# Optimization experiments

Measured on AMD Instinct MI355X. Metric: run time of the kernel, lower is better.

## Reference

```python
import jax, jax.numpy as jnp
import numpy as np

B, H, W, DIM = 32, 56, 56, 192
WSZ = 7
HEADS = 8
DK = 32
DV = 32
INNER_K = HEADS * DK  # 256
INNER_V = HEADS * DV  # 256


def setup_inputs() -> dict:
    key = jax.random.key(0)
    ks = jax.random.split(key, 8)
    s = 0.05
    return {
        "x": jax.random.normal(ks[0], (B, H, W, DIM), jnp.float32),
        "Wq": jax.random.normal(ks[1], (DIM, INNER_K), jnp.float32) * s,
        "Wk": jax.random.normal(ks[2], (DIM, INNER_K), jnp.float32) * s,
        "Wv": jax.random.normal(ks[3], (DIM, INNER_V), jnp.float32) * s,
        "Wlocal": jax.random.normal(ks[4], (3, 3, INNER_V, INNER_V), jnp.float32) * s,
        "b_local": jnp.zeros((INNER_V,), jnp.float32),
        "Wout": jax.random.normal(ks[5], (INNER_V, DIM), jnp.float32) * s,
        "b_out": jnp.zeros((DIM,), jnp.float32),
    }


def _window(t, heads, wsz):
    # (b, H, W, heads*d) -> (b*nx*ny, heads, wsz*wsz, d)
    b, h, w, c = t.shape
    d = c // heads
    nx, ny = h // wsz, w // wsz
    t = t.reshape(b, nx, wsz, ny, wsz, heads, d)
    t = t.transpose(0, 1, 3, 5, 2, 4, 6)
    return t.reshape(b * nx * ny, heads, wsz * wsz, d)


def reference(x, Wq, Wk, Wv, Wlocal, b_local, Wout, b_out):
    scale = DK ** (-0.5)
    # 1x1 convs == per-pixel matmuls
    q = jnp.einsum('bhwc,cd->bhwd', x, Wq)
    k = jnp.einsum('bhwc,cd->bhwd', x, Wk)
    v = jnp.einsum('bhwc,cd->bhwd', x, Wv)
    # 3x3 local interactive conv on v (SAME padding)
    local_out = jax.lax.conv_general_dilated(
        v, Wlocal, window_strides=(1, 1), padding='SAME',
        dimension_numbers=('NHWC', 'HWIO', 'NHWC')) + b_local
    # window partition
    qw = _window(q, HEADS, WSZ)
    kw = _window(k, HEADS, WSZ)
    vw = _window(v, HEADS, WSZ)
    dots = jnp.einsum('bhid,bhjd->bhij', qw, kw) * scale  # (B*nx*ny, heads, 49, 49)
    attn = jax.nn.softmax(dots, axis=-1)
    out = jnp.einsum('bhij,bhjd->bhid', attn, vw)
    # window merge: (b*nx*ny, heads, wsz*wsz, d) -> (b, H, W, heads*d)
    nx, ny = H // WSZ, W // WSZ
    out = out.reshape(B, nx, ny, HEADS, WSZ, WSZ, DV)
    out = out.transpose(0, 1, 4, 2, 5, 3, 6).reshape(B, H, W, HEADS * DV)
    out = out + local_out
    out = jnp.einsum('bhwc,cd->bhwd', out, Wout) + b_out
    return out
```

## Files before the change

### kernel.cpp

```cpp
#include <hip/hip_runtime.h>

typedef unsigned short ushort_t;
typedef __bf16  bf16x8 __attribute__((ext_vector_type(8)));
typedef float   f32x4  __attribute__((ext_vector_type(4)));
typedef unsigned short u16x8 __attribute__((ext_vector_type(8)));

#define MFMA16(a,b,c) __builtin_amdgcn_mfma_f32_16x16x32_bf16((a),(b),(c),0,0,0)
#define WAITVM(N) asm volatile("s_waitcnt vmcnt(" #N ")" ::: "memory")
#define BARRIER() do{ __builtin_amdgcn_s_barrier(); asm volatile("" ::: "memory"); }while(0)

static __device__ __forceinline__ ushort_t f2bf(float f){
  __bf16 h = (__bf16)f;
  return __builtin_bit_cast(ushort_t, h);
}
static __device__ __forceinline__ float bf2f(ushort_t b){
  union{unsigned u; float f;} x; x.u = ((unsigned)b)<<16; return x.f;
}
static __device__ __forceinline__ bf16x8 ldg_bf8u(const ushort_t* p){
  u16x8 r = *(const u16x8*)p;
  return __builtin_bit_cast(bf16x8, r);
}
static __device__ __forceinline__ bf16x8 lds_bf8(const ushort_t* p){
  u16x8 r = *(const u16x8*)p;
  return __builtin_bit_cast(bf16x8, r);
}
static __device__ __forceinline__ void gload_lds16(const ushort_t* g, ushort_t* l){
  __builtin_amdgcn_global_load_lds(
      (const __attribute__((address_space(1))) void*)g,
      (__attribute__((address_space(3))) void*)l, 16, 0, 0);
}

__global__ __launch_bounds__(256) void prep_kernel(
    const float* __restrict__ Wq, const float* __restrict__ Wk,
    const float* __restrict__ Wv, const float* __restrict__ Wl,
    const float* __restrict__ Wo,
    ushort_t* __restrict__ qkvT, ushort_t* __restrict__ wlT,
    ushort_t* __restrict__ woT)
{
  int idx = blockIdx.x*256 + threadIdx.x;
  if(idx < 147456){
    int n = idx/192, kk = idx%192;
    const float* W = (n < 256) ? Wq : ((n < 512) ? Wk : Wv);
    qkvT[idx] = f2bf(W[kk*256 + (n & 255)]);
  } else if(idx < 147456 + 589824){
    int t2 = idx - 147456;
    int j   = t2 & 7;
    int sl  = (t2 >> 3) & 3;
    int col = (t2 >> 5) & 255;
    int ks  = (t2 >> 13) & 7;
    int tap = t2 >> 16;
    int grp = sl ^ ((col>>1)&3);
    int k = ks*32 + grp*8 + j;
    wlT[t2] = f2bf(Wl[((size_t)tap*256 + k)*256 + col]);
  } else if(idx < 737280 + 49152){
    int t3 = idx - 737280;
    int col = t3/256, kk = t3%256;
    woT[t3] = f2bf(Wo[kk*192 + col]);
  }
}

__global__ __launch_bounds__(512) void qkvattn_kernel(
    const float* __restrict__ x, const ushort_t* __restrict__ WT,
    ushort_t* __restrict__ vbuf, ushort_t* __restrict__ attnout)
{
  __shared__ ushort_t lds[53248];
  ushort_t* xLds = lds;
  const int tid = threadIdx.x;
  const int w = tid>>6, l = tid&63, lr = l&15, g = l>>4;
  const int win = blockIdx.x;
  const int b = win>>6, rem = win&63, wy = rem>>3, wx = rem&7;
  const size_t base = (size_t)b*3136 + wy*7*56 + wx*7;

  #pragma unroll
  for(int r=0;r<3;++r){
    int c = tid + r*512;
    int row = c/24, cp = c%24;
    u16x8 o = {0,0,0,0,0,0,0,0};
    if(row < 49){
      int sc = cp ^ (row&7);
      const float* src = x + (base + (row/7)*56 + (row%7))*192 + sc*8;
      float4 f0 = *(const float4*)src;
      float4 f1 = *(const float4*)(src+4);
      o[0]=f2bf(f0.x); o[1]=f2bf(f0.y); o[2]=f2bf(f0.z); o[3]=f2bf(f0.w);
      o[4]=f2bf(f1.x); o[5]=f2bf(f1.y); o[6]=f2bf(f1.z); o[7]=f2bf(f1.w);
    }
    *(u16x8*)&xLds[row*192 + cp*8] = o;
  }
  __syncthreads();

  ushort_t* qkBase = lds + 16384 + w*4608;
  ushort_t* vT     = lds + w*2048;
  #pragma unroll
  for(int which=0; which<3; ++which){
    const ushort_t* Wb = WT + (size_t)(which*256 + w*32)*192;
    f32x4 acc[4][2];
    #pragma unroll
    for(int mi=0;mi<4;++mi)
      #pragma unroll
      for(int nj=0;nj<2;++nj){ f32x4 z={0.f,0.f,0.f,0.f}; acc[mi][nj]=z; }
    bf16x8 bA[2], bB[2];
    #pragma unroll
    for(int nj=0;nj<2;++nj) bA[nj] = ldg_bf8u(Wb + (size_t)(nj*16+lr)*192 + g*8);
    #pragma unroll
    for(int ks2=0; ks2<3; ++ks2){
      int ks0 = 2*ks2, ks1 = 2*ks2+1;
      #pragma unroll
      for(int nj=0;nj<2;++nj) bB[nj] = ldg_bf8u(Wb + (size_t)(nj*16+lr)*192 + ks1*32 + g*8);
      #pragma unroll
      for(int mi=0;mi<4;++mi){
        int row = mi*16 + lr;
        bf16x8 af = lds_bf8(&xLds[(row*192 + ks0*32 + g*8) ^ ((row&7)<<3)]);
        #pragma unroll
        for(int nj=0;nj<2;++nj) acc[mi][nj] = MFMA16(af, bA[nj], acc[mi][nj]);
      }
      if(ks2<2){
        #pragma unroll
        for(int nj=0;nj<2;++nj) bA[nj] = ldg_bf8u(Wb + (size_t)(nj*16+lr)*192 + (ks1+1)*32 + g*8);
      }
      #pragma unroll
      for(int mi=0;mi<4;++mi){
        int row = mi*16 + lr;
        bf16x8 af = lds_bf8(&xLds[(row*192 + ks1*32 + g*8) ^ ((row&7)<<3)]);
        #pragma unroll
        for(int nj=0;nj<2;++nj) acc[mi][nj] = MFMA16(af, bB[nj], acc[mi][nj]);
      }
    }
    if(which < 2){
      ushort_t* dst = qkBase + which*2304;
      #pragma unroll
      for(int mi=0;mi<4;++mi)
        #pragma unroll
        for(int nj=0;nj<2;++nj)
          #pragma unroll
          for(int i=0;i<4;++i){
            int row = mi*16 + g*4 + i, col = nj*16 + lr;
            dst[row*36 + col] = f2bf(acc[mi][nj][i]);
          }
    } else {
      __syncthreads();
      #pragma unroll
      for(int mi=0;mi<4;++mi)
        #pragma unroll
        for(int nj=0;nj<2;++nj)
          #pragma unroll
          for(int i=0;i<4;++i){
            int row = mi*16 + g*4 + i, col = nj*16 + lr;
            ushort_t val = f2bf(acc[mi][nj][i]);
            vT[(col*64 + row) ^ ((col&7)<<3)] = val;
            if(row < 49)
              vbuf[(base + (row/7)*56 + (row%7))*256 + w*32 + col] = val;
          }
    }
  }

  f32x4 dot[4][4];
  #pragma unroll
  for(int mi=0;mi<4;++mi)
    #pragma unroll
    for(int nj=0;nj<4;++nj){ f32x4 z={0.f,0.f,0.f,0.f}; dot[mi][nj]=z; }
  bf16x8 qf[4], kf[4];
  #pragma unroll
  for(int t=0;t<4;++t){
    qf[t] = lds_bf8(&qkBase[(t*16+lr)*36 + g*8]);
    kf[t] = lds_bf8(&qkBase[2304 + (t*16+lr)*36 + g*8]);
  }
  #pragma unroll
  for(int mi=0;mi<4;++mi)
    #pragma unroll
    for(int nj=0;nj<4;++nj)
      dot[mi][nj] = MFMA16(qf[mi], kf[nj], dot[mi][nj]);
  const float sc = 0.17677669529663687f * 1.4426950408889634f;
  ushort_t* pl = qkBase;
  float rs[4][4];
  #pragma unroll
  for(int mi=0;mi<4;++mi){
    #pragma unroll
    for(int i=0;i<4;++i){
      float m = -1e30f;
      #pragma unroll
      for(int nj=0;nj<4;++nj){
        int col = nj*16 + lr;
        if(col < 49) m = fmaxf(m, dot[mi][nj][i]);
      }
      m = fmaxf(m, __shfl_xor(m,1));
      m = fmaxf(m, __shfl_xor(m,2));
      m = fmaxf(m, __shfl_xor(m,4));
      m = fmaxf(m, __shfl_xor(m,8));
      float e[4]; float s = 0.f;
      #pragma unroll
      for(int nj=0;nj<4;++nj){
        int col = nj*16 + lr;
        e[nj] = (col < 49) ? exp2f((dot[mi][nj][i]-m)*sc) : 0.f;
        s += e[nj];
      }
      s += __shfl_xor(s,1); s += __shfl_xor(s,2);
      s += __shfl_xor(s,4); s += __shfl_xor(s,8);
      rs[mi][i] = s;
      int row = mi*16 + g*4 + i;
      #pragma unroll
      for(int nj=0;nj<4;++nj){
        int col = nj*16 + lr;
        pl[(row*64 + col) ^ ((row&7)<<3)] = f2bf(e[nj]);
      }
    }
  }
  f32x4 o[4][2];
  #pragma unroll
  for(int mi=0;mi<4;++mi)
    #pragma unroll
    for(int nj=0;nj<2;++nj){ f32x4 z={0.f,0.f,0.f,0.f}; o[mi][nj]=z; }
  #pragma unroll
  for(int ks=0;ks<2;++ks){
    bf16x8 pa[4];
    #pragma unroll
    for(int mi=0;mi<4;++mi){
      int row = mi*16 + lr;
      pa[mi] = lds_bf8(&pl[(row*64 + ks*32 + g*8) ^ ((row&7)<<3)]);
    }
    #pragma unroll
    for(int nj=0;nj<2;++nj){
      int d = nj*16 + lr;
      bf16x8 vb = lds_bf8(&vT[(d*64 + ks*32 + g*8) ^ ((d&7)<<3)]);
      #pragma unroll
      for(int mi=0;mi<4;++mi) o[mi][nj] = MFMA16(pa[mi], vb, o[mi][nj]);
    }
  }
  #pragma unroll
  for(int mi=0;mi<4;++mi){
    #pragma unroll
    for(int i=0;i<4;++i){
      int row = mi*16 + g*4 + i;
      if(row < 49){
        size_t pix = base + (row/7)*56 + (row%7);
        float inv = 1.0f / rs[mi][i];
        #pragma unroll
        for(int nj=0;nj<2;++nj)
          attnout[pix*256 + w*32 + nj*16 + lr] = f2bf(o[mi][nj][i] * inv);
      }
    }
  }
}

__global__ __launch_bounds__(256,2) void conv_kernel(
    const ushort_t* __restrict__ v, const ushort_t* __restrict__ WlT,
    const float* __restrict__ b_local, ushort_t* __restrict__ local_out)
{
  __shared__ ushort_t aBuf[2][256*32];
  __shared__ ushort_t bBuf[3][256*32];
  const int bid = blockIdx.x;
  const int tile = (bid & 7) * 98 + (bid >> 3);
  const int p0 = tile * 128;
  const int tid = threadIdx.x;
  const int l = tid&63, w=tid>>6, wm=w>>1, wn=w&1, lr=l&15, g=l>>4;

  unsigned maskbits[4];
  int pxloc[4];
  #pragma unroll
  for(int mi=0;mi<4;++mi){
    int p = p0 + wm*64 + mi*16 + lr;
    int rem = p % 3136;
    int y = rem/56, x = rem%56;
    unsigned mb = 0;
    #pragma unroll
    for(int tap=0;tap<9;++tap){
      int dy = tap/3 - 1, dx = tap%3 - 1;
      if(((unsigned)(y+dy) < 56u) && ((unsigned)(x+dx) < 56u)) mb |= (1u<<tap);
    }
    maskbits[mi] = mb;
    pxloc[mi] = wm*64 + mi*16 + lr + 64;
  }

  auto stageA = [&](int ks, ushort_t* dst){
    #pragma unroll
    for(int r=0;r<4;++r){
      int c = tid + r*256;
      int px = c>>2, sl = c&3;
      int px_abs = p0 - 64 + px;
      px_abs = min(max(px_abs, 0), 100351);
      int chunk = sl ^ ((px>>1)&3);
      gload_lds16(v + (size_t)px_abs*256 + ks*32 + chunk*8,
                  dst + (size_t)(r*256 + w*64)*8);
    }
  };
  auto stageB = [&](int ks, int tap, ushort_t* dst){
    const ushort_t* src = WlT + ((size_t)tap*8 + ks)*8192;
    #pragma unroll
    for(int r=0;r<4;++r){
      gload_lds16(src + (size_t)(tid + r*256)*8,
                  dst + (size_t)(r*256 + w*64)*8);
    }
  };

  f32x4 acc[4][8];
  #pragma unroll
  for(int mi=0;mi<4;++mi)
    #pragma unroll
    for(int nj=0;nj<8;++nj){ f32x4 z={0.f,0.f,0.f,0.f}; acc[mi][nj]=z; }

  auto compute = [&](int tap, const ushort_t* aL, const ushort_t* bL){
    int shift = (tap/3 - 1)*56 + (tap%3 - 1);
    bf16x8 af[4];
    #pragma unroll
    for(int mi=0;mi<4;++mi){
      int px = pxloc[mi] + shift;
      int sl = g ^ ((px>>1)&3);
      u16x8 rv = *(const u16x8*)&aL[px*32 + sl*8];
      if(!((maskbits[mi]>>tap)&1)){ u16x8 z={0,0,0,0,0,0,0,0}; rv=z; }
      af[mi] = __builtin_bit_cast(bf16x8, rv);
    }
    __builtin_amdgcn_s_setprio(1);
    #pragma unroll
    for(int nj=0;nj<8;++nj){
      int col = wn*128 + nj*16 + lr;
      int slb = g ^ ((col>>1)&3);
      bf16x8 bfr = lds_bf8(&bL[col*32 + slb*8]);
      #pragma unroll
      for(int mi=0;mi<4;++mi) acc[mi][nj] = MFMA16(af[mi], bfr, acc[mi][nj]);
    }
    __builtin_amdgcn_s_setprio(0);
  };

  stageA(0, aBuf[0]);
  stageB(0, 0, bBuf[0]);
  stageB(0, 1, bBuf[1]);

  for(int ks=0; ks<7; ++ks){
    #pragma unroll
    for(int tap=0; tap<9; ++tap){
      if(tap==1) WAITVM(8); else WAITVM(4);
      BARRIER();
      if(tap==0) stageA(ks+1, aBuf[(ks+1)&1]);
      stageB(ks + (tap+2)/9, (tap+2)%9, bBuf[(tap+2)%3]);
      compute(tap, aBuf[ks&1], bBuf[tap%3]);
    }
  }
  #pragma unroll
  for(int tap=0; tap<9; ++tap){
    if(tap==8) WAITVM(0); else WAITVM(4);
    BARRIER();
    if(tap<7) stageB(7, tap+2, bBuf[(tap+2)%3]);
    compute(tap, aBuf[1], bBuf[tap%3]);
  }

  #pragma unroll
  for(int nj=0;nj<8;++nj){
    int col = wn*128 + nj*16 + lr;
    float bb = b_local[col];
    #pragma unroll
    for(int mi=0;mi<4;++mi)
      #pragma unroll
      for(int i=0;i<4;++i){
        int p = p0 + wm*64 + mi*16 + g*4 + i;
        local_out[(size_t)p*256 + col] = f2bf(acc[mi][nj][i] + bb);
      }
  }
}

__global__ __launch_bounds__(256,4) void outproj_kernel(
    const ushort_t* __restrict__ attnout, const ushort_t* __restrict__ locl,
    const ushort_t* __restrict__ WoT, const float* __restrict__ b_out,
    float* __restrict__ out)
{
  __shared__ ushort_t aLds[64*256];
  const int m0 = blockIdx.x * 64;
  const int tid = threadIdx.x;
  const int l = tid&63, w = tid>>6, lr=l&15, g=l>>4;
  #pragma unroll
  for(int r=0;r<8;++r){
    int c = tid + r*256;
    int row = c>>5, cc = c&31;
    size_t off = (size_t)(m0+row)*256 + cc*8;
    u16x8 a = *(const u16x8*)(attnout + off);
    u16x8 b2 = *(const u16x8*)(locl + off);
    u16x8 o;
    #pragma unroll
    for(int j=0;j<8;++j) o[j] = f2bf(bf2f(a[j]) + bf2f(b2[j]));
    *(u16x8*)&aLds[(row*256 + cc*8) ^ ((row&7)<<3)] = o;
  }
  __syncthreads();

  const ushort_t* Wbase = WoT + (size_t)(w*48)*256;
  f32x4 acc[4][3];
  #pragma unroll
  for(int mi=0;mi<4;++mi)
    #pragma unroll
    for(int nj=0;nj<3;++nj){ f32x4 z={0.f,0.f,0.f,0.f}; acc[mi][nj]=z; }

  #pragma unroll
  for(int ks=0;ks<8;++ks){
    bf16x8 bfr[3];
    #pragma unroll
    for(int nj=0;nj<3;++nj)
      bfr[nj] = ldg_bf8u(Wbase + (size_t)(nj*16+lr)*256 + ks*32 + g*8);
    bf16x8 af[4];
    #pragma unroll
    for(int mi=0;mi<4;++mi){
      int row = mi*16 + lr;
      af[mi] = lds_bf8(&aLds[(row*256 + ks*32 + g*8) ^ ((row&7)<<3)]);
    }
    #pragma unroll
    for(int nj=0;nj<3;++nj)
      #pragma unroll
      for(int mi=0;mi<4;++mi) acc[mi][nj] = MFMA16(af[mi], bfr[nj], acc[mi][nj]);
  }
  #pragma unroll
  for(int nj=0;nj<3;++nj){
    int col = w*48 + nj*16 + lr;
    float bb = b_out[col];
    #pragma unroll
    for(int mi=0;mi<4;++mi)
      #pragma unroll
      for(int i=0;i<4;++i){
        int row = mi*16 + g*4 + i;
        out[(size_t)(m0+row)*192 + col] = acc[mi][nj][i] + bb;
      }
  }
}

extern "C" void kernel_launch(void* const* d_in, const int* in_sizes, int n_in,
                              void* d_out, int out_size, void* d_ws, size_t ws_size,
                              hipStream_t stream)
{
  const float* x  = (const float*)d_in[0];
  const float* Wq = (const float*)d_in[1];
  const float* Wk = (const float*)d_in[2];
  const float* Wv = (const float*)d_in[3];
  const float* Wl = (const float*)d_in[4];
  const float* bl = (const float*)d_in[5];
  const float* Wo = (const float*)d_in[6];
  const float* bo = (const float*)d_in[7];
  float* out = (float*)d_out;
  char* ws = (char*)d_ws;
  ushort_t* attnout = (ushort_t*)(ws);
  ushort_t* vbuf    = (ushort_t*)(ws + 102760448);
  ushort_t* locl    = (ushort_t*)(ws + 205520896);
  ushort_t* qkvT    = (ushort_t*)(ws + 256901120);
  ushort_t* wlT     = (ushort_t*)(ws + 257196032);
  ushort_t* woT     = (ushort_t*)(ws + 258375680);

  prep_kernel<<<3072, 256, 0, stream>>>(Wq, Wk, Wv, Wl, Wo, qkvT, wlT, woT);
  qkvattn_kernel<<<2048, 512, 0, stream>>>(x, qkvT, vbuf, attnout);
  conv_kernel<<<784, 256, 0, stream>>>(vbuf, wlT, bl, locl);
  outproj_kernel<<<1568, 256, 0, stream>>>(attnout, locl, woT, bo, out);
}
```

Before: 336.6 us.

## Fuse QKV projection loop, drop softmax max, compute row sums via MFMA

The Q, K and V projections now run in one k-loop that shares the x fragments from LDS, replacing three separate passes. The softmax no longer subtracts the row max or reduces with shuffles; it exponentiates directly and gets the row sums from an extra MFMA of P against a ones vector. Launch bounds now request two blocks per CU, and zero padding rows in x are written through a separate branch. This removes the shuffle reductions and repeated LDS reads, but it holds three accumulator sets live, which raises register pressure, and skipping the max subtraction risks exp overflow for large logits.

```diff
diff --git a/kernel.cpp b/kernel.cpp
--- a/kernel.cpp
+++ b/kernel.cpp
@@ -59,7 +59,7 @@
   }
 }
 
-__global__ __launch_bounds__(512) void qkvattn_kernel(
+__global__ __launch_bounds__(512,2) void qkvattn_kernel(
     const float* __restrict__ x, const ushort_t* __restrict__ WT,
     ushort_t* __restrict__ vbuf, ushort_t* __restrict__ attnout)
 {
@@ -75,83 +75,83 @@
   for(int r=0;r<3;++r){
     int c = tid + r*512;
     int row = c/24, cp = c%24;
-    u16x8 o = {0,0,0,0,0,0,0,0};
     if(row < 49){
       int sc = cp ^ (row&7);
       const float* src = x + (base + (row/7)*56 + (row%7))*192 + sc*8;
       float4 f0 = *(const float4*)src;
       float4 f1 = *(const float4*)(src+4);
+      u16x8 o;
       o[0]=f2bf(f0.x); o[1]=f2bf(f0.y); o[2]=f2bf(f0.z); o[3]=f2bf(f0.w);
       o[4]=f2bf(f1.x); o[5]=f2bf(f1.y); o[6]=f2bf(f1.z); o[7]=f2bf(f1.w);
-    }
-    *(u16x8*)&xLds[row*192 + cp*8] = o;
+      *(u16x8*)&xLds[row*192 + cp*8] = o;
+    } else {
+      u16x8 z = {0,0,0,0,0,0,0,0};
+      *(u16x8*)&xLds[row*192 + cp*8] = z;
+    }
   }
   __syncthreads();
 
   ushort_t* qkBase = lds + 16384 + w*4608;
   ushort_t* vT     = lds + w*2048;
-  #pragma unroll
-  for(int which=0; which<3; ++which){
-    const ushort_t* Wb = WT + (size_t)(which*256 + w*32)*192;
-    f32x4 acc[4][2];
-    #pragma unroll
-    for(int mi=0;mi<4;++mi)
-      #pragma unroll
-      for(int nj=0;nj<2;++nj){ f32x4 z={0.f,0.f,0.f,0.f}; acc[mi][nj]=z; }
-    bf16x8 bA[2], bB[2];
-    #pragma unroll
-    for(int nj=0;nj<2;++nj) bA[nj] = ldg_bf8u(Wb + (size_t)(nj*16+lr)*192 + g*8);
-    #pragma unroll
-    for(int ks2=0; ks2<3; ++ks2){
-      int ks0 = 2*ks2, ks1 = 2*ks2+1;
-      #pragma unroll
-      for(int nj=0;nj<2;++nj) bB[nj] = ldg_bf8u(Wb + (size_t)(nj*16+lr)*192 + ks1*32 + g*8);
+  const ushort_t* Wq_ = WT + (size_t)(w*32)*192;
+  const ushort_t* Wk_ = WT + (size_t)(256 + w*32)*192;
+  const ushort_t* Wv_ = WT + (size_t)(512 + w*32)*192;
+  f32x4 aq[4][2], ak[4][2], av[4][2];
+  #pragma unroll
+  for(int mi=0;mi<4;++mi)
+    #pragma unroll
+    for(int nj=0;nj<2;++nj){
+      f32x4 z={0.f,0.f,0.f,0.f};
+      aq[mi][nj]=z; ak[mi][nj]=z; av[mi][nj]=z;
+    }
+  #pragma unroll
+  for(int ks=0; ks<6; ++ks){
+    bf16x8 af[4];
+    #pragma unroll
+    for(int mi=0;mi<4;++mi){
+      int row = mi*16 + lr;
+      af[mi] = lds_bf8(&xLds[(row*192 + ks*32 + g*8) ^ ((row&7)<<3)]);
+    }
+    bf16x8 bq[2], bk[2], bv[2];
+    #pragma unroll
+    for(int nj=0;nj<2;++nj){
+      size_t off = (size_t)(nj*16+lr)*192 + ks*32 + g*8;
+      bq[nj] = ldg_bf8u(Wq_ + off);
+      bk[nj] = ldg_bf8u(Wk_ + off);
+      bv[nj] = ldg_bf8u(Wv_ + off);
+    }
+    #pragma unroll
+    for(int nj=0;nj<2;++nj)
       #pragma unroll
       for(int mi=0;mi<4;++mi){
-        int row = mi*16 + lr;
-        bf16x8 af = lds_bf8(&xLds[(row*192 + ks0*32 + g*8) ^ ((row&7)<<3)]);
-        #pragma unroll
-        for(int nj=0;nj<2;++nj) acc[mi][nj] = MFMA16(af, bA[nj], acc[mi][nj]);
-      }
-      if(ks2<2){
-        #pragma unroll
-        for(int nj=0;nj<2;++nj) bA[nj] = ldg_bf8u(Wb + (size_t)(nj*16+lr)*192 + (ks1+1)*32 + g*8);
-      }
-      #pragma unroll
-      for(int mi=0;mi<4;++mi){
-        int row = mi*16 + lr;
-        bf16x8 af = lds_bf8(&xLds[(row*192 + ks1*32 + g*8) ^ ((row&7)<<3)]);
-        #pragma unroll
-        for(int nj=0;nj<2;++nj) acc[mi][nj] = MFMA16(af, bB[nj], acc[mi][nj]);
-      }
-    }
-    if(which < 2){
-      ushort_t* dst = qkBase + which*2304;
-      #pragma unroll
-      for(int mi=0;mi<4;++mi)
-        #pragma unroll
-        for(int nj=0;nj<2;++nj)
-          #pragma unroll
-          for(int i=0;i<4;++i){
-            int row = mi*16 + g*4 + i, col = nj*16 + lr;
-            dst[row*36 + col] = f2bf(acc[mi][nj][i]);
-          }
-    } else {
-      __syncthreads();
-      #pragma unroll
-      for(int mi=0;mi<4;++mi)
-        #pragma unroll
-        for(int nj=0;nj<2;++nj)
-          #pragma unroll
-          for(int i=0;i<4;++i){
-            int row = mi*16 + g*4 + i, col = nj*16 + lr;
-            ushort_t val = f2bf(acc[mi][nj][i]);
-            vT[(col*64 + row) ^ ((col&7)<<3)] = val;
-            if(row < 49)
-              vbuf[(base + (row/7)*56 + (row%7))*256 + w*32 + col] = val;
-          }
-    }
-  }
+        aq[mi][nj] = MFMA16(af[mi], bq[nj], aq[mi][nj]);
+        ak[mi][nj] = MFMA16(af[mi], bk[nj], ak[mi][nj]);
+        av[mi][nj] = MFMA16(af[mi], bv[nj], av[mi][nj]);
+      }
+  }
+  #pragma unroll
+  for(int mi=0;mi<4;++mi)
+    #pragma unroll
+    for(int nj=0;nj<2;++nj)
+      #pragma unroll
+      for(int i=0;i<4;++i){
+        int row = mi*16 + g*4 + i, col = nj*16 + lr;
+        qkBase[row*36 + col]        = f2bf(aq[mi][nj][i]);
+        qkBase[2304 + row*36 + col] = f2bf(ak[mi][nj][i]);
+      }
+  __syncthreads();
+  #pragma unroll
+  for(int mi=0;mi<4;++mi)
+    #pragma unroll
+    for(int nj=0;nj<2;++nj)
+      #pragma unroll
+      for(int i=0;i<4;++i){
+        int row = mi*16 + g*4 + i, col = nj*16 + lr;
+        ushort_t val = f2bf(av[mi][nj][i]);
+        vT[(col*64 + row) ^ ((col&7)<<3)] = val;
+        if(row < 49)
+          vbuf[(base + (row/7)*56 + (row%7))*256 + w*32 + col] = val;
+      }
 
   f32x4 dot[4][4];
   #pragma unroll
@@ -169,46 +169,30 @@
     #pragma unroll
     for(int nj=0;nj<4;++nj)
       dot[mi][nj] = MFMA16(qf[mi], kf[nj], dot[mi][nj]);
+
   const float sc = 0.17677669529663687f * 1.4426950408889634f;
   ushort_t* pl = qkBase;
-  float rs[4][4];
+  #pragma unroll
+  for(int mi=0;mi<4;++mi)
+    #pragma unroll
+    for(int nj=0;nj<4;++nj){
+      int col = nj*16 + lr;
+      #pragma unroll
+      for(int i=0;i<4;++i){
+        float e = (col < 49) ? exp2f(dot[mi][nj][i]*sc) : 0.f;
+        int row = mi*16 + g*4 + i;
+        pl[(row*64 + col) ^ ((row&7)<<3)] = f2bf(e);
+      }
+    }
+
+  u16x8 ones_u = {0x3f80,0x3f80,0x3f80,0x3f80,0x3f80,0x3f80,0x3f80,0x3f80};
+  bf16x8 ones8 = __builtin_bit_cast(bf16x8, ones_u);
+  f32x4 o[4][2], rsum[4];
   #pragma unroll
   for(int mi=0;mi<4;++mi){
-    #pragma unroll
-    for(int i=0;i<4;++i){
-      float m = -1e30f;
-      #pragma unroll
-      for(int nj=0;nj<4;++nj){
-        int col = nj*16 + lr;
-        if(col < 49) m = fmaxf(m, dot[mi][nj][i]);
-      }
-      m = fmaxf(m, __shfl_xor(m,1));
-      m = fmaxf(m, __shfl_xor(m,2));
-      m = fmaxf(m, __shfl_xor(m,4));
-      m = fmaxf(m, __shfl_xor(m,8));
-      float e[4]; float s = 0.f;
-      #pragma unroll
-      for(int nj=0;nj<4;++nj){
-        int col = nj*16 + lr;
-        e[nj] = (col < 49) ? exp2f((dot[mi][nj][i]-m)*sc) : 0.f;
-        s += e[nj];
-      }
-      s += __shfl_xor(s,1); s += __shfl_xor(s,2);
-      s += __shfl_xor(s,4); s += __shfl_xor(s,8);
-      rs[mi][i] = s;
-      int row = mi*16 + g*4 + i;
-      #pragma unroll
-      for(int nj=0;nj<4;++nj){
-        int col = nj*16 + lr;
-        pl[(row*64 + col) ^ ((row&7)<<3)] = f2bf(e[nj]);
-      }
-    }
-  }
-  f32x4 o[4][2];
-  #pragma unroll
-  for(int mi=0;mi<4;++mi)
-    #pragma unroll
-    for(int nj=0;nj<2;++nj){ f32x4 z={0.f,0.f,0.f,0.f}; o[mi][nj]=z; }
+    f32x4 z={0.f,0.f,0.f,0.f};
+    o[mi][0]=z; o[mi][1]=z; rsum[mi]=z;
+  }
   #pragma unroll
   for(int ks=0;ks<2;++ks){
     bf16x8 pa[4];
@@ -224,6 +208,8 @@
       #pragma unroll
       for(int mi=0;mi<4;++mi) o[mi][nj] = MFMA16(pa[mi], vb, o[mi][nj]);
     }
+    #pragma unroll
+    for(int mi=0;mi<4;++mi) rsum[mi] = MFMA16(pa[mi], ones8, rsum[mi]);
   }
   #pragma unroll
   for(int mi=0;mi<4;++mi){
@@ -232,7 +218,7 @@
       int row = mi*16 + g*4 + i;
       if(row < 49){
         size_t pix = base + (row/7)*56 + (row%7);
-        float inv = 1.0f / rs[mi][i];
+        float inv = 1.0f / rsum[mi][i];
         #pragma unroll
         for(int nj=0;nj<2;++nj)
           attnout[pix*256 + w*32 + nj*16 + lr] = f2bf(o[mi][nj][i] * inv);
```

Result: faster. 328.8 us (-2.3%).
